# Kernel optimization log

Hardware: AMD Instinct MI355X
Metric: run time of the kernel (lower is better)

The kernel has to match this reference:

```python
import jax, jax.numpy as jnp
import numpy as np

N = 100000   # nodes
E = 640000   # edges
IN = 256     # raw input feature dim
D = 128      # post-MLP node feature dim (fixed in FilterGNN)


def setup_inputs() -> dict:
    key = jax.random.key(0)
    ks = jax.random.split(key, 10)
    x = jax.random.normal(ks[0], (N, IN), jnp.float32)
    alpha = jax.random.uniform(ks[1], (E, 1), jnp.float32)  # edge gate logits in [0,1)
    edge_index = jax.random.randint(ks[2], (2, E), 0, N, dtype=jnp.int32)
    norm = jnp.ones((E,), jnp.float32)  # passed to message in the original but unused
    # MLP `lin`: in_channels -> 512 -> 256 -> 128 (kaiming-normal weights, zero bias)
    def kaiming(k, fan_out, fan_in):
        return jax.random.normal(k, (fan_out, fan_in), jnp.float32) * jnp.sqrt(2.0 / fan_in)
    W1 = kaiming(ks[3], 512, IN); b1 = jnp.zeros((512,), jnp.float32)
    W2 = kaiming(ks[4], 256, 512); b2 = jnp.zeros((256,), jnp.float32)
    W3 = kaiming(ks[5], D, 256);  b3 = jnp.zeros((D,), jnp.float32)
    return {"x": x, "alpha": alpha, "edge_index": edge_index, "norm": norm,
            "W1": W1, "b1": b1, "W2": W2, "b2": b2, "W3": W3, "b3": b3}


def reference(x, alpha, edge_index, norm, W1, b1, W2, b2, W3, b3):
    # FilterGNN.lin: Linear-Tanh-Linear-Tanh-Linear  -> [N, 128]
    h = jnp.tanh(x @ W1.T + b1)
    h = jnp.tanh(h @ W2.T + b2)
    h = h @ W3.T + b3
    # FilterGraphConv1: gather x_j, elementwise relu gate, scatter-mean over targets.
    # (The [-1, H, C] view with H*C = 128 is a pure reshape; the gate broadcasts
    #  over all features, so the math is identical without the head split.)
    src, dst = edge_index[0], edge_index[1]
    gate = 2.0 * jax.nn.relu(jax.lax.stop_gradient(alpha) - 0.5)  # [E, 1]
    msg = h[src] * gate                                           # [E, 128] gather + gate
    sums = jax.ops.segment_sum(msg, dst, num_segments=N)          # [N, 128]
    cnt = jax.ops.segment_sum(jnp.ones((E,), h.dtype), dst, num_segments=N)
    out = sums / jnp.maximum(cnt, 1.0)[:, None]                   # scatter-mean (0 if no edges)
    return out
```

## Files before the change

### kernel.cpp

```cpp
#include <hip/hip_runtime.h>

typedef __attribute__((ext_vector_type(8))) short short8;
typedef __attribute__((ext_vector_type(4))) float f32x4;

__device__ __forceinline__ unsigned short f2bf(float f) {
    union { float f; unsigned u; } v; v.f = f;
    unsigned r = v.u + 0x7FFFu + ((v.u >> 16) & 1u);
    return (unsigned short)(r >> 16);
}
__device__ __forceinline__ float bf2f(unsigned short h) {
    union { unsigned u; float f; } v; v.u = ((unsigned)h) << 16;
    return v.f;
}

__device__ __forceinline__ float tanh_fast(float x) {
    float xc = fminf(fmaxf(x, -9.0f), 9.0f);
    float t  = __expf(2.0f * xc);
    return (t - 1.0f) * __builtin_amdgcn_rcpf(t + 1.0f);
}

#define GLD16(gptr, lptr)                                                     \
    __builtin_amdgcn_global_load_lds(                                         \
        (const __attribute__((address_space(1))) unsigned int*)(gptr),        \
        (__attribute__((address_space(3))) unsigned int*)(lptr), 16, 0, 0)

__device__ __forceinline__ unsigned pk_trunc(float lo, float hi) {
    return __builtin_amdgcn_perm(__float_as_uint(hi), __float_as_uint(lo), 0x07060302u);
}

__global__ __launch_bounds__(256) void cast_weights(
    const float* __restrict__ W1, const float* __restrict__ W2,
    const float* __restrict__ W3, unsigned short* __restrict__ w1bf,
    unsigned short* __restrict__ w2bf, unsigned short* __restrict__ w3bf)
{
    int t = (blockIdx.x * 256 + threadIdx.x) * 4;
    const float* s; unsigned short* d; int base;
    if (t < 131072)      { s = W1; d = w1bf; base = t; }
    else if (t < 262144) { s = W2; d = w2bf; base = t - 131072; }
    else if (t < 294912) { s = W3; d = w3bf; base = t - 262144; }
    else return;
    float4 v = *(const float4*)(s + base);
    unsigned long long p =
        (unsigned long long)f2bf(v.x)
      | ((unsigned long long)f2bf(v.y) << 16)
      | ((unsigned long long)f2bf(v.z) << 32)
      | ((unsigned long long)f2bf(v.w) << 48);
    *(unsigned long long*)(d + base) = p;
}

#define TM 128
#define TN 128
#define BK 64

__global__ __launch_bounds__(256) void gemm_a32_bt(
    const float* __restrict__ A, const unsigned short* __restrict__ B,
    const float* __restrict__ bias, unsigned short* __restrict__ C,
    int M, int N, int K)
{
    __shared__ __align__(16) float Asf[TM][BK];
    __shared__ __align__(16) short Bs[TM][BK];

    const int tid  = threadIdx.x;
    const int wave = tid >> 6;
    const int lane = tid & 63;
    const int m0 = blockIdx.x * TM;
    const int n0 = blockIdx.y * TN;
    const int wm = (wave >> 1) * 64;
    const int wn = (wave & 1) * 64;
    const int lm = lane & 15;
    const int quad = lane >> 4;

    const int srowA = lane >> 4;
    const int lA    = lane & 15;
    const int srowB = lane >> 3;
    const int cB    = ((lane & 7) ^ srowB) * 8;

    f32x4 acc[4][4] = {};

    for (int k0 = 0; k0 < K; k0 += BK) {
        #pragma unroll
        for (int i = 0; i < 8; ++i) {
            int row0 = wave * 32 + i * 4;
            int gr = m0 + row0 + srowA; if (gr >= M) gr = M - 1;
            int cA = lA ^ ((row0 + srowA) & 15);
            GLD16(A + (size_t)gr * K + k0 + cA * 4, &Asf[row0][0]);
        }
        #pragma unroll
        for (int i = 0; i < 4; ++i) {
            int row0 = wave * 32 + i * 8;
            GLD16(B + (size_t)(n0 + row0 + srowB) * K + k0 + cB, &Bs[row0][0]);
        }
        __syncthreads();

        #pragma unroll
        for (int ks = 0; ks < BK; ks += 32) {
            const int qb = ks >> 2;
            const int ccB = (((ks >> 3) + quad) ^ (lm & 7)) * 8;
            short8 af[4], bfr[4];
            #pragma unroll
            for (int i = 0; i < 4; ++i) {
                const float* rowp = &Asf[wm + i * 16 + lm][0];
                float4 f0 = *(const float4*)(rowp + (((qb + quad * 2)     ) ^ lm) * 4);
                float4 f1 = *(const float4*)(rowp + (((qb + quad * 2) + 1) ^ lm) * 4);
                union { short8 s; uint4 u; } cv;
                cv.u.x = pk_trunc(f0.x, f0.y);
                cv.u.y = pk_trunc(f0.z, f0.w);
                cv.u.z = pk_trunc(f1.x, f1.y);
                cv.u.w = pk_trunc(f1.z, f1.w);
                af[i]  = cv.s;
                bfr[i] = *(const short8*)&Bs[wn + i * 16 + lm][ccB];
            }
            #pragma unroll
            for (int im = 0; im < 4; ++im)
                #pragma unroll
                for (int in = 0; in < 4; ++in)
                    acc[im][in] = __builtin_amdgcn_mfma_f32_16x16x32_bf16(
                        af[im], bfr[in], acc[im][in], 0, 0, 0);
        }
        __syncthreads();
    }

    #pragma unroll
    for (int im = 0; im < 4; ++im) {
        int gm_base = m0 + wm + im * 16 + quad * 4;
        #pragma unroll
        for (int in = 0; in < 4; ++in) {
            int gn = n0 + wn + in * 16 + lm;
            float bv = bias[gn];
            #pragma unroll
            for (int r = 0; r < 4; ++r) {
                int gm = gm_base + r;
                if (gm < M) {
                    float v = tanh_fast(acc[im][in][r] + bv);
                    C[(size_t)gm * N + gn] = f2bf(v);
                }
            }
        }
    }
}

template<bool TANH>
__global__ __launch_bounds__(256) void gemm_bt(
    const unsigned short* __restrict__ A, const unsigned short* __restrict__ B,
    const float* __restrict__ bias, unsigned short* __restrict__ C,
    int M, int N, int K)
{
    __shared__ __align__(16) short As[TM][BK];
    __shared__ __align__(16) short Bs[TM][BK];

    const int tid  = threadIdx.x;
    const int wave = tid >> 6;
    const int lane = tid & 63;
    const int m0 = blockIdx.x * TM;
    const int n0 = blockIdx.y * TN;
    const int wm = (wave >> 1) * 64;
    const int wn = (wave & 1) * 64;
    const int lm = lane & 15;
    const int quad = lane >> 4;

    const int srow = lane >> 3;
    const int scol = ((lane & 7) ^ srow) * 8;
    const int cc0 = (quad ^ (lm & 7)) * 8;
    const int cc1 = ((4 + quad) ^ (lm & 7)) * 8;

    f32x4 acc[4][4] = {};

    for (int k0 = 0; k0 < K; k0 += BK) {
        #pragma unroll
        for (int i = 0; i < 4; ++i) {
            int row = wave * 32 + i * 8;
            int gr = m0 + row + srow; if (gr >= M) gr = M - 1;
            GLD16(A + (size_t)gr * K + k0 + scol, &As[row][0]);
            GLD16(B + (size_t)(n0 + row + srow) * K + k0 + scol, &Bs[row][0]);
        }
        __syncthreads();

        #pragma unroll
        for (int ks = 0; ks < BK; ks += 32) {
            const int cc = (ks == 0) ? cc0 : cc1;
            short8 af[4], bf_[4];
            #pragma unroll
            for (int i = 0; i < 4; ++i) {
                af[i]  = *(const short8*)&As[wm + i * 16 + lm][cc];
                bf_[i] = *(const short8*)&Bs[wn + i * 16 + lm][cc];
            }
            #pragma unroll
            for (int im = 0; im < 4; ++im)
                #pragma unroll
                for (int in = 0; in < 4; ++in)
                    acc[im][in] = __builtin_amdgcn_mfma_f32_16x16x32_bf16(
                        af[im], bf_[in], acc[im][in], 0, 0, 0);
        }
        __syncthreads();
    }

    #pragma unroll
    for (int im = 0; im < 4; ++im) {
        int gm_base = m0 + wm + im * 16 + quad * 4;
        #pragma unroll
        for (int in = 0; in < 4; ++in) {
            int gn = n0 + wn + in * 16 + lm;
            float bv = bias[gn];
            #pragma unroll
            for (int r = 0; r < 4; ++r) {
                int gm = gm_base + r;
                if (gm < M) {
                    float v = acc[im][in][r] + bv;
                    if (TANH) v = tanh_fast(v);
                    C[(size_t)gm * N + gn] = f2bf(v);
                }
            }
        }
    }
}

__global__ __launch_bounds__(256) void edge_hist(
    const int* __restrict__ ei, const float* __restrict__ alpha,
    unsigned long long* __restrict__ deg, int E)
{
    int e = blockIdx.x * 256 + threadIdx.x;
    if (e >= E) return;
    int dst = ei[E + e];
    float gate = 2.0f * fmaxf(alpha[e] - 0.5f, 0.0f);
    atomicAdd(&deg[dst], 0x100000000ULL | (gate > 0.0f ? 1ULL : 0ULL));
}

__global__ __launch_bounds__(256) void scan1(
    const unsigned long long* __restrict__ deg, int* __restrict__ rowptr,
    int* __restrict__ cursor, int* __restrict__ partials, int N)
{
    __shared__ int sums[256];
    int base = blockIdx.x * 1024 + threadIdx.x * 4;
    int v[4];
    #pragma unroll
    for (int i = 0; i < 4; ++i) {
        int idx = base + i;
        v[i] = (idx < N) ? (int)(deg[idx] & 0xffffffffULL) : 0;
    }
    int s = v[0] + v[1] + v[2] + v[3];
    sums[threadIdx.x] = s;
    __syncthreads();
    for (int off = 1; off < 256; off <<= 1) {
        int t = (threadIdx.x >= off) ? sums[threadIdx.x - off] : 0;
        __syncthreads();
        sums[threadIdx.x] += t;
        __syncthreads();
    }
    int excl = sums[threadIdx.x] - s;
    if (threadIdx.x == 255) partials[blockIdx.x] = sums[255];
    int run = excl;
    #pragma unroll
    for (int i = 0; i < 4; ++i) {
        int idx = base + i;
        if (idx < N) { rowptr[idx] = run; cursor[idx] = run; }
        run += v[i];
    }
}

__global__ __launch_bounds__(256) void scan2(int* __restrict__ partials, int nb)
{
    __shared__ int s[256];
    int v = (threadIdx.x < nb) ? partials[threadIdx.x] : 0;
    s[threadIdx.x] = v;
    __syncthreads();
    for (int off = 1; off < 256; off <<= 1) {
        int t = (threadIdx.x >= off) ? s[threadIdx.x - off] : 0;
        __syncthreads();
        s[threadIdx.x] += t;
        __syncthreads();
    }
    partials[threadIdx.x] = s[threadIdx.x] - v;
}

__global__ __launch_bounds__(256) void edge_fill(
    const int* __restrict__ ei, const float* __restrict__ alpha,
    int* __restrict__ cursor, const int* __restrict__ partials,
    int2* __restrict__ recs, int E)
{
    int e = blockIdx.x * 256 + threadIdx.x;
    if (e >= E) return;
    float gate = 2.0f * fmaxf(alpha[e] - 0.5f, 0.0f);
    if (gate > 0.0f) {
        int dst = ei[E + e];
        int src = ei[e];
        int pos = atomicAdd(&cursor[dst], 1) + partials[dst >> 10];
        recs[pos] = make_int2(src, __float_as_int(gate));
    }
}

__global__ __launch_bounds__(256) void node_gather(
    const unsigned short* __restrict__ h, const unsigned long long* __restrict__ deg,
    const int* __restrict__ rowptr, const int* __restrict__ partials,
    const int2* __restrict__ recs, float* __restrict__ out, int N)
{
    int wave = threadIdx.x >> 6;
    int lane = threadIdx.x & 63;
    int node = blockIdx.x * 4 + wave;
    if (node >= N) return;
    unsigned long long d = deg[node];
    int dAll  = __builtin_amdgcn_readfirstlane((int)(d >> 32));
    int dG    = __builtin_amdgcn_readfirstlane((int)(d & 0xffffffffULL));
    int start = __builtin_amdgcn_readfirstlane(rowptr[node] + partials[node >> 10]);
    int half = lane >> 5, hl = lane & 31;
    float ax = 0.f, ay = 0.f, az = 0.f, aw = 0.f;
    for (int j = 0; j < dG; j += 2) {
        int jj = j + half;
        int idx = start + (jj < dG ? jj : dG - 1);
        int2 rec = recs[idx];
        float gate = (jj < dG) ? __int_as_float(rec.y) : 0.0f;
        uint2 u = *(const uint2*)(h + ((size_t)rec.x << 7) + hl * 4);
        ax += bf2f((unsigned short)(u.x & 0xffffu)) * gate;
        ay += bf2f((unsigned short)(u.x >> 16)) * gate;
        az += bf2f((unsigned short)(u.y & 0xffffu)) * gate;
        aw += bf2f((unsigned short)(u.y >> 16)) * gate;
    }
    ax += __shfl_down(ax, 32);
    ay += __shfl_down(ay, 32);
    az += __shfl_down(az, 32);
    aw += __shfl_down(aw, 32);
    if (half == 0) {
        float inv = 1.0f / fmaxf((float)dAll, 1.0f);
        *(float4*)(out + ((size_t)node << 7) + hl * 4) =
            make_float4(ax * inv, ay * inv, az * inv, aw * inv);
    }
}

extern "C" void kernel_launch(void* const* d_in, const int* in_sizes, int n_in,
                              void* d_out, int out_size, void* d_ws, size_t ws_size,
                              hipStream_t stream) {
    const float* x     = (const float*)d_in[0];
    const float* alpha = (const float*)d_in[1];
    const int*   ei    = (const int*)d_in[2];
    const float* W1 = (const float*)d_in[4];
    const float* b1 = (const float*)d_in[5];
    const float* W2 = (const float*)d_in[6];
    const float* b2 = (const float*)d_in[7];
    const float* W3 = (const float*)d_in[8];
    const float* b3 = (const float*)d_in[9];
    float* out = (float*)d_out;

    const int N = in_sizes[0] / 256;
    const int E = in_sizes[1];
    const int IN = 256, H1 = 512, H2 = 256, D = 128;

    char* ws = (char*)d_ws;
    size_t off = 0;
    auto take = [&](size_t bytes) { char* p = ws + off; off = (off + bytes + 255) & ~(size_t)255; return p; };
    unsigned short* h1bf = (unsigned short*)take((size_t)N * H1 * 2);
    unsigned short* h2bf = (unsigned short*)take((size_t)N * H2 * 2);
    unsigned short* hbf  = (unsigned short*)take((size_t)N * D  * 2);
    unsigned short* w1bf = (unsigned short*)take((size_t)H1 * IN * 2);
    unsigned short* w2bf = (unsigned short*)take((size_t)H2 * H1 * 2);
    unsigned short* w3bf = (unsigned short*)take((size_t)D  * H2 * 2);

    char* cbase = (char*)h1bf;
    size_t coff = 0;
    auto ctake = [&](size_t bytes) { char* p = cbase + coff; coff = (coff + bytes + 255) & ~(size_t)255; return p; };
    unsigned long long* deg = (unsigned long long*)ctake((size_t)N * 8);
    int*  rowptr   = (int*)ctake((size_t)N * 4);
    int*  cursor   = (int*)ctake((size_t)N * 4);
    int*  partials = (int*)ctake(256 * 4);
    int2* recs     = (int2*)ctake((size_t)E * 8);

    dim3 blk(256);

    cast_weights<<<(294912 / 4 + 255) / 256, blk, 0, stream>>>(W1, W2, W3, w1bf, w2bf, w3bf);

    const int mblk = (N + TM - 1) / TM;
    gemm_a32_bt    <<<dim3(mblk, H1 / TN), blk, 0, stream>>>(x,    w1bf, b1, h1bf, N, H1, IN);
    gemm_bt<true > <<<dim3(mblk, H2 / TN), blk, 0, stream>>>(h1bf, w2bf, b2, h2bf, N, H2, H1);
    gemm_bt<false> <<<dim3(mblk, D / TN),  blk, 0, stream>>>(h2bf, w3bf, b3, hbf,  N, D,  H2);

    hipMemsetAsync(deg, 0, (size_t)N * 8, stream);
    edge_hist<<<(E + 255) / 256, blk, 0, stream>>>(ei, alpha, deg, E);
    const int nb1 = (N + 1023) / 1024;
    scan1<<<nb1, blk, 0, stream>>>(deg, rowptr, cursor, partials, N);
    scan2<<<1, blk, 0, stream>>>(partials, nb1);
    edge_fill<<<(E + 255) / 256, blk, 0, stream>>>(ei, alpha, cursor, partials, recs, E);

    node_gather<<<(N + 3) / 4, blk, 0, stream>>>(hbf, deg, rowptr, partials, recs, out, N);
}
```

Measured before the change: 441.1 us.

## Pre-cast x to bf16, fuse layers 2 and 3, widen gather loads

Layer 1 now works from a bf16 copy of x made in one combined cast kernel, so the fp32 A tile and its in-loop conversion disappear from the GEMM. Layers 2 and 3 are fused into one kernel that keeps the 64x256 h2 tile in LDS, avoiding the write and re-read of h2 through global memory and one launch. The gather kernel moves to 16-byte loads, with four edges processed per wave. In exchange x is read and written an extra time, and the fused kernel uses a large LDS footprint (about 74 KB) that may cut occupancy; it also reloads the full W2 tile for every 64-row block.

```diff
diff --git a/kernel.cpp b/kernel.cpp
--- a/kernel.cpp
+++ b/kernel.cpp
@@ -24,21 +24,24 @@
         (const __attribute__((address_space(1))) unsigned int*)(gptr),        \
         (__attribute__((address_space(3))) unsigned int*)(lptr), 16, 0, 0)
 
-__device__ __forceinline__ unsigned pk_trunc(float lo, float hi) {
-    return __builtin_amdgcn_perm(__float_as_uint(hi), __float_as_uint(lo), 0x07060302u);
-}
-
-__global__ __launch_bounds__(256) void cast_weights(
-    const float* __restrict__ W1, const float* __restrict__ W2,
-    const float* __restrict__ W3, unsigned short* __restrict__ w1bf,
-    unsigned short* __restrict__ w2bf, unsigned short* __restrict__ w3bf)
-{
-    int t = (blockIdx.x * 256 + threadIdx.x) * 4;
-    const float* s; unsigned short* d; int base;
-    if (t < 131072)      { s = W1; d = w1bf; base = t; }
-    else if (t < 262144) { s = W2; d = w2bf; base = t - 131072; }
-    else if (t < 294912) { s = W3; d = w3bf; base = t - 262144; }
-    else return;
+__global__ __launch_bounds__(256) void cast_all(
+    const float* __restrict__ x,  unsigned short* __restrict__ xbf,
+    const float* __restrict__ W1, unsigned short* __restrict__ w1bf,
+    const float* __restrict__ W2, unsigned short* __restrict__ w2bf,
+    const float* __restrict__ W3, unsigned short* __restrict__ w3bf,
+    int xq)
+{
+    int t = blockIdx.x * 256 + threadIdx.x;
+    const float* s; unsigned short* d; int q;
+    if (t < xq) { s = x; d = xbf; q = t; }
+    else {
+        int u = t - xq;
+        if (u < 32768)      { s = W1; d = w1bf; q = u; }
+        else if (u < 65536) { s = W2; d = w2bf; q = u - 32768; }
+        else if (u < 73728) { s = W3; d = w3bf; q = u - 65536; }
+        else return;
+    }
+    int base = q * 4;
     float4 v = *(const float4*)(s + base);
     unsigned long long p =
         (unsigned long long)f2bf(v.x)
@@ -52,12 +55,12 @@
 #define TN 128
 #define BK 64
 
-__global__ __launch_bounds__(256) void gemm_a32_bt(
-    const float* __restrict__ A, const unsigned short* __restrict__ B,
+__global__ __launch_bounds__(256) void gemm_bt(
+    const unsigned short* __restrict__ A, const unsigned short* __restrict__ B,
     const float* __restrict__ bias, unsigned short* __restrict__ C,
     int M, int N, int K)
 {
-    __shared__ __align__(16) float Asf[TM][BK];
+    __shared__ __align__(16) short As[TM][BK];
     __shared__ __align__(16) short Bs[TM][BK];
 
     const int tid  = threadIdx.x;
@@ -70,52 +73,38 @@
     const int lm = lane & 15;
     const int quad = lane >> 4;
 
-    const int srowA = lane >> 4;
-    const int lA    = lane & 15;
-    const int srowB = lane >> 3;
-    const int cB    = ((lane & 7) ^ srowB) * 8;
+    const int srow = lane >> 3;
+    const int scol = ((lane & 7) ^ srow) * 8;
+    const int cc0 = (quad ^ (lm & 7)) * 8;
+    const int cc1 = ((4 + quad) ^ (lm & 7)) * 8;
 
     f32x4 acc[4][4] = {};
 
     for (int k0 = 0; k0 < K; k0 += BK) {
         #pragma unroll
-        for (int i = 0; i < 8; ++i) {
-            int row0 = wave * 32 + i * 4;
-            int gr = m0 + row0 + srowA; if (gr >= M) gr = M - 1;
-            int cA = lA ^ ((row0 + srowA) & 15);
-            GLD16(A + (size_t)gr * K + k0 + cA * 4, &Asf[row0][0]);
-        }
-        #pragma unroll
         for (int i = 0; i < 4; ++i) {
-            int row0 = wave * 32 + i * 8;
-            GLD16(B + (size_t)(n0 + row0 + srowB) * K + k0 + cB, &Bs[row0][0]);
+            int row = wave * 32 + i * 8;
+            int gr = m0 + row + srow; if (gr >= M) gr = M - 1;
+            GLD16(A + (size_t)gr * K + k0 + scol, &As[row][0]);
+            GLD16(B + (size_t)(n0 + row + srow) * K + k0 + scol, &Bs[row][0]);
         }
         __syncthreads();
 
         #pragma unroll
         for (int ks = 0; ks < BK; ks += 32) {
-            const int qb = ks >> 2;
-            const int ccB = (((ks >> 3) + quad) ^ (lm & 7)) * 8;
-            short8 af[4], bfr[4];
+            const int cc = (ks == 0) ? cc0 : cc1;
+            short8 af[4], bf_[4];
             #pragma unroll
             for (int i = 0; i < 4; ++i) {
-                const float* rowp = &Asf[wm + i * 16 + lm][0];
-                float4 f0 = *(const float4*)(rowp + (((qb + quad * 2)     ) ^ lm) * 4);
-                float4 f1 = *(const float4*)(rowp + (((qb + quad * 2) + 1) ^ lm) * 4);
-                union { short8 s; uint4 u; } cv;
-                cv.u.x = pk_trunc(f0.x, f0.y);
-                cv.u.y = pk_trunc(f0.z, f0.w);
-                cv.u.z = pk_trunc(f1.x, f1.y);
-                cv.u.w = pk_trunc(f1.z, f1.w);
-                af[i]  = cv.s;
-                bfr[i] = *(const short8*)&Bs[wn + i * 16 + lm][ccB];
+                af[i]  = *(const short8*)&As[wm + i * 16 + lm][cc];
+                bf_[i] = *(const short8*)&Bs[wn + i * 16 + lm][cc];
             }
             #pragma unroll
             for (int im = 0; im < 4; ++im)
                 #pragma unroll
                 for (int in = 0; in < 4; ++in)
                     acc[im][in] = __builtin_amdgcn_mfma_f32_16x16x32_bf16(
-                        af[im], bfr[in], acc[im][in], 0, 0, 0);
+                        af[im], bf_[in], acc[im][in], 0, 0, 0);
         }
         __syncthreads();
     }
@@ -139,75 +128,117 @@
     }
 }
 
-template<bool TANH>
-__global__ __launch_bounds__(256) void gemm_bt(
-    const unsigned short* __restrict__ A, const unsigned short* __restrict__ B,
-    const float* __restrict__ bias, unsigned short* __restrict__ C,
-    int M, int N, int K)
-{
-    __shared__ __align__(16) short As[TM][BK];
-    __shared__ __align__(16) short Bs[TM][BK];
+__global__ __launch_bounds__(256) void gemm23(
+    const unsigned short* __restrict__ h1, const unsigned short* __restrict__ W2,
+    const float* __restrict__ b2, const unsigned short* __restrict__ W3,
+    const float* __restrict__ b3, unsigned short* __restrict__ hout, int M)
+{
+    __shared__ __align__(16) short As[64][64];
+    __shared__ __align__(16) short Bs[256][64];
+    __shared__ __align__(16) short h2s[64][264];
 
     const int tid  = threadIdx.x;
     const int wave = tid >> 6;
     const int lane = tid & 63;
-    const int m0 = blockIdx.x * TM;
-    const int n0 = blockIdx.y * TN;
-    const int wm = (wave >> 1) * 64;
-    const int wn = (wave & 1) * 64;
+    const int m0 = blockIdx.x * 64;
+    const int wm = (wave >> 1) * 32;
     const int lm = lane & 15;
     const int quad = lane >> 4;
-
     const int srow = lane >> 3;
     const int scol = ((lane & 7) ^ srow) * 8;
     const int cc0 = (quad ^ (lm & 7)) * 8;
     const int cc1 = ((4 + quad) ^ (lm & 7)) * 8;
 
-    f32x4 acc[4][4] = {};
-
-    for (int k0 = 0; k0 < K; k0 += BK) {
+    {
+        const int wn = (wave & 1) * 128;
+        f32x4 acc[2][8] = {};
+        for (int k0 = 0; k0 < 512; k0 += 64) {
+            #pragma unroll
+            for (int i = 0; i < 2; ++i) {
+                int r0 = wave * 16 + i * 8;
+                int gr = m0 + r0 + srow; if (gr >= M) gr = M - 1;
+                GLD16(h1 + (size_t)gr * 512 + k0 + scol, &As[r0][0]);
+            }
+            #pragma unroll
+            for (int i = 0; i < 8; ++i) {
+                int r0 = wave * 64 + i * 8;
+                GLD16(W2 + (size_t)(r0 + srow) * 512 + k0 + scol, &Bs[r0][0]);
+            }
+            __syncthreads();
+            #pragma unroll
+            for (int ks = 0; ks < 64; ks += 32) {
+                const int cc = (ks == 0) ? cc0 : cc1;
+                short8 af[2], bf_[8];
+                #pragma unroll
+                for (int i = 0; i < 2; ++i) af[i]  = *(const short8*)&As[wm + i * 16 + lm][cc];
+                #pragma unroll
+                for (int i = 0; i < 8; ++i) bf_[i] = *(const short8*)&Bs[wn + i * 16 + lm][cc];
+                #pragma unroll
+                for (int im = 0; im < 2; ++im)
+                    #pragma unroll
+                    for (int in = 0; in < 8; ++in)
+                        acc[im][in] = __builtin_amdgcn_mfma_f32_16x16x32_bf16(
+                            af[im], bf_[in], acc[im][in], 0, 0, 0);
+            }
+            __syncthreads();
+        }
         #pragma unroll
-        for (int i = 0; i < 4; ++i) {
-            int row = wave * 32 + i * 8;
-            int gr = m0 + row + srow; if (gr >= M) gr = M - 1;
-            GLD16(A + (size_t)gr * K + k0 + scol, &As[row][0]);
-            GLD16(B + (size_t)(n0 + row + srow) * K + k0 + scol, &Bs[row][0]);
-        }
-        __syncthreads();
-
+        for (int im = 0; im < 2; ++im) {
+            int rb = wm + im * 16 + quad * 4;
+            #pragma unroll
+            for (int in = 0; in < 8; ++in) {
+                int col = wn + in * 16 + lm;
+                float bv = b2[col];
+                #pragma unroll
+                for (int r = 0; r < 4; ++r)
+                    h2s[rb + r][col] = (short)f2bf(tanh_fast(acc[im][in][r] + bv));
+            }
+        }
+    }
+    __syncthreads();
+
+    {
+        const int wn = (wave & 1) * 64;
+        short (*Bs3)[64] = (short(*)[64])&Bs[0][0];
+        f32x4 acc[2][4] = {};
+        for (int k0 = 0; k0 < 256; k0 += 64) {
+            #pragma unroll
+            for (int i = 0; i < 4; ++i) {
+                int r0 = wave * 32 + i * 8;
+                GLD16(W3 + (size_t)(r0 + srow) * 256 + k0 + scol, &Bs3[r0][0]);
+            }
+            __syncthreads();
+            #pragma unroll
+            for (int ks = 0; ks < 64; ks += 32) {
+                const int cc = (ks == 0) ? cc0 : cc1;
+                short8 af[2], bf_[4];
+                #pragma unroll
+                for (int i = 0; i < 2; ++i)
+                    af[i] = *(const short8*)&h2s[wm + i * 16 + lm][k0 + ks + quad * 8];
+                #pragma unroll
+                for (int i = 0; i < 4; ++i)
+                    bf_[i] = *(const short8*)&Bs3[wn + i * 16 + lm][cc];
+                #pragma unroll
+                for (int im = 0; im < 2; ++im)
+                    #pragma unroll
+                    for (int in = 0; in < 4; ++in)
+                        acc[im][in] = __builtin_amdgcn_mfma_f32_16x16x32_bf16(
+                            af[im], bf_[in], acc[im][in], 0, 0, 0);
+            }
+            __syncthreads();
+        }
         #pragma unroll
-        for (int ks = 0; ks < BK; ks += 32) {
-            const int cc = (ks == 0) ? cc0 : cc1;
-            short8 af[4], bf_[4];
-            #pragma unroll
-            for (int i = 0; i < 4; ++i) {
-                af[i]  = *(const short8*)&As[wm + i * 16 + lm][cc];
-                bf_[i] = *(const short8*)&Bs[wn + i * 16 + lm][cc];
-            }
-            #pragma unroll
-            for (int im = 0; im < 4; ++im)
-                #pragma unroll
-                for (int in = 0; in < 4; ++in)
-                    acc[im][in] = __builtin_amdgcn_mfma_f32_16x16x32_bf16(
-                        af[im], bf_[in], acc[im][in], 0, 0, 0);
-        }
-        __syncthreads();
-    }
-
-    #pragma unroll
-    for (int im = 0; im < 4; ++im) {
-        int gm_base = m0 + wm + im * 16 + quad * 4;
-        #pragma unroll
-        for (int in = 0; in < 4; ++in) {
-            int gn = n0 + wn + in * 16 + lm;
-            float bv = bias[gn];
-            #pragma unroll
-            for (int r = 0; r < 4; ++r) {
-                int gm = gm_base + r;
-                if (gm < M) {
-                    float v = acc[im][in][r] + bv;
-                    if (TANH) v = tanh_fast(v);
-                    C[(size_t)gm * N + gn] = f2bf(v);
+        for (int im = 0; im < 2; ++im) {
+            int gm_base = m0 + wm + im * 16 + quad * 4;
+            #pragma unroll
+            for (int in = 0; in < 4; ++in) {
+                int gn = wn + in * 16 + lm;
+                float bv = b3[gn];
+                #pragma unroll
+                for (int r = 0; r < 4; ++r) {
+                    int gm = gm_base + r;
+                    if (gm < M)
+                        hout[(size_t)gm * 128 + gn] = f2bf(acc[im][in][r] + bv);
                 }
             }
         }
@@ -301,27 +332,33 @@
     int dAll  = __builtin_amdgcn_readfirstlane((int)(d >> 32));
     int dG    = __builtin_amdgcn_readfirstlane((int)(d & 0xffffffffULL));
     int start = __builtin_amdgcn_readfirstlane(rowptr[node] + partials[node >> 10]);
-    int half = lane >> 5, hl = lane & 31;
-    float ax = 0.f, ay = 0.f, az = 0.f, aw = 0.f;
-    for (int j = 0; j < dG; j += 2) {
-        int jj = j + half;
+    int qw = lane >> 4, ql = lane & 15;
+    float a[8] = {};
+    for (int j = 0; j < dG; j += 4) {
+        int jj = j + qw;
         int idx = start + (jj < dG ? jj : dG - 1);
         int2 rec = recs[idx];
         float gate = (jj < dG) ? __int_as_float(rec.y) : 0.0f;
-        uint2 u = *(const uint2*)(h + ((size_t)rec.x << 7) + hl * 4);
-        ax += bf2f((unsigned short)(u.x & 0xffffu)) * gate;
-        ay += bf2f((unsigned short)(u.x >> 16)) * gate;
-        az += bf2f((unsigned short)(u.y & 0xffffu)) * gate;
-        aw += bf2f((unsigned short)(u.y >> 16)) * gate;
-    }
-    ax += __shfl_down(ax, 32);
-    ay += __shfl_down(ay, 32);
-    az += __shfl_down(az, 32);
-    aw += __shfl_down(aw, 32);
-    if (half == 0) {
+        uint4 u = *(const uint4*)(h + ((size_t)rec.x << 7) + ql * 8);
+        a[0] += bf2f((unsigned short)(u.x & 0xffffu)) * gate;
+        a[1] += bf2f((unsigned short)(u.x >> 16)) * gate;
+        a[2] += bf2f((unsigned short)(u.y & 0xffffu)) * gate;
+        a[3] += bf2f((unsigned short)(u.y >> 16)) * gate;
+        a[4] += bf2f((unsigned short)(u.z & 0xffffu)) * gate;
+        a[5] += bf2f((unsigned short)(u.z >> 16)) * gate;
+        a[6] += bf2f((unsigned short)(u.w & 0xffffu)) * gate;
+        a[7] += bf2f((unsigned short)(u.w >> 16)) * gate;
+    }
+    #pragma unroll
+    for (int i = 0; i < 8; ++i) {
+        a[i] += __shfl_xor(a[i], 16);
+        a[i] += __shfl_xor(a[i], 32);
+    }
+    if (qw == 0) {
         float inv = 1.0f / fmaxf((float)dAll, 1.0f);
-        *(float4*)(out + ((size_t)node << 7) + hl * 4) =
-            make_float4(ax * inv, ay * inv, az * inv, aw * inv);
+        float* op = out + ((size_t)node << 7) + ql * 8;
+        *(float4*)(op)     = make_float4(a[0] * inv, a[1] * inv, a[2] * inv, a[3] * inv);
+        *(float4*)(op + 4) = make_float4(a[4] * inv, a[5] * inv, a[6] * inv, a[7] * inv);
     }
 }
 
@@ -341,17 +378,17 @@
 
     const int N = in_sizes[0] / 256;
     const int E = in_sizes[1];
-    const int IN = 256, H1 = 512, H2 = 256, D = 128;
+    const int IN = 256, H1 = 512, D = 128;
 
     char* ws = (char*)d_ws;
     size_t off = 0;
     auto take = [&](size_t bytes) { char* p = ws + off; off = (off + bytes + 255) & ~(size_t)255; return p; };
+    unsigned short* xbf  = (unsigned short*)take((size_t)N * IN * 2);
     unsigned short* h1bf = (unsigned short*)take((size_t)N * H1 * 2);
-    unsigned short* h2bf = (unsigned short*)take((size_t)N * H2 * 2);
     unsigned short* hbf  = (unsigned short*)take((size_t)N * D  * 2);
     unsigned short* w1bf = (unsigned short*)take((size_t)H1 * IN * 2);
-    unsigned short* w2bf = (unsigned short*)take((size_t)H2 * H1 * 2);
-    unsigned short* w3bf = (unsigned short*)take((size_t)D  * H2 * 2);
+    unsigned short* w2bf = (unsigned short*)take((size_t)256 * H1 * 2);
+    unsigned short* w3bf = (unsigned short*)take((size_t)D * 256 * 2);
 
     char* cbase = (char*)h1bf;
     size_t coff = 0;
@@ -364,12 +401,13 @@
 
     dim3 blk(256);
 
-    cast_weights<<<(294912 / 4 + 255) / 256, blk, 0, stream>>>(W1, W2, W3, w1bf, w2bf, w3bf);
+    const int xq = N * IN / 4;
+    const int castN = xq + 73728;
+    cast_all<<<(castN + 255) / 256, blk, 0, stream>>>(x, xbf, W1, w1bf, W2, w2bf, W3, w3bf, xq);
 
     const int mblk = (N + TM - 1) / TM;
-    gemm_a32_bt    <<<dim3(mblk, H1 / TN), blk, 0, stream>>>(x,    w1bf, b1, h1bf, N, H1, IN);
-    gemm_bt<true > <<<dim3(mblk, H2 / TN), blk, 0, stream>>>(h1bf, w2bf, b2, h2bf, N, H2, H1);
-    gemm_bt<false> <<<dim3(mblk, D / TN),  blk, 0, stream>>>(h2bf, w3bf, b3, hbf,  N, D,  H2);
+    gemm_bt<<<dim3(mblk, H1 / TN), blk, 0, stream>>>(xbf, w1bf, b1, h1bf, N, H1, IN);
+    gemm23<<<(N + 63) / 64, blk, 0, stream>>>(h1bf, w2bf, b2, w3bf, b3, hbf, N);
 
     hipMemsetAsync(deg, 0, (size_t)N * 8, stream);
     edge_hist<<<(E + 255) / 256, blk, 0, stream>>>(ei, alpha, deg, E);
```

After: 410.9 us. -6.8%, faster.
